# Performance work log

Measured on AMD Instinct MI355X. Metric: run time of the kernel, lower is better.

The kernel has to match this reference:

```python
import jax, jax.numpy as jnp
import numpy as np

EPS = 1e-5   # torch F.layer_norm default eps
TOP_K = 20   # int(3*D^2 / (2*hr*N^2 + 10*D)) for D=768, N=196, hr=1.0
NUM_EXPERTS = 200  # 10 * TOP_K


def setup_inputs() -> dict:
    key = jax.random.key(0)
    ks = jax.random.split(key, 6)
    B, N, D = 32, 196, 768
    E, H = NUM_EXPERTS, 196  # H = int(N * hidden_ratio)
    s = 0.02
    return {
        "x": jax.random.normal(ks[0], (B, N, D), jnp.float32),
        "Wr": jax.random.normal(ks[1], (E, D), jnp.float32) * s,   # router.weight
        "W1": jax.random.normal(ks[2], (E, H, N), jnp.float32) * s,  # fc1.weight per expert
        "b1": jnp.zeros((E, H), jnp.float32),
        "W2": jax.random.normal(ks[3], (E, N, H), jnp.float32) * s,  # fc2.weight per expert
        "b2": jnp.zeros((E, N), jnp.float32),
        "Wo": jax.random.normal(ks[4], (D, D), jnp.float32) * s,     # out_proj.weight
        "bo": jnp.zeros((D,), jnp.float32),
    }


def reference(x, Wr, W1, b1, W2, b2, Wo, bo):
    B, N, D = x.shape
    E = Wr.shape[0]
    K = TOP_K

    # Router: per-sample routing on token-mean features
    logits = x.mean(axis=1) @ Wr.T                      # (B, E)
    probs = jax.nn.softmax(logits, axis=-1)             # (B, E)
    w, idx = jax.lax.top_k(probs, K)                    # (B, K) sorted desc, as torch.topk
    w = w / w.sum(axis=-1, keepdims=True)               # renormalize top-k weights

    # TokenMixer operates in (B, D, N) space: layernorm over tokens (no affine),
    # then fc1 (N->H), gelu(tanh), fc2 (H->N).
    xt = jnp.swapaxes(x, 1, 2)                          # (B, D, N)
    mu = xt.mean(axis=-1, keepdims=True)
    var = xt.var(axis=-1, keepdims=True)                # population var (matches F.layer_norm)
    z = (xt - mu) * jax.lax.rsqrt(var + EPS)            # (B, D, N)

    # Gather each sample's K expert weight matrices and batch the MLPs.
    W1g, b1g = W1[idx], b1[idx]                         # (B,K,H,N), (B,K,H)
    W2g, b2g = W2[idx], b2[idx]                         # (B,K,N,H), (B,K,N)

    h = jnp.einsum('bdn,bkhn->bkdh', z, W1g) + b1g[:, :, None, :]
    a = jax.nn.gelu(h, approximate=True)                # tanh-approx GELU
    o = jnp.einsum('bkdh,bknh->bkdn', a, W2g) + b2g[:, :, None, :]

    # Weighted combine over the K selected experts, back to (B, N, D)
    mix = jnp.einsum('bk,bkdn->bnd', w, o)

    out = mix @ Wo.T + bo                               # out_proj

    # Load-balancing aux loss (top-1 assignment fraction vs mean router prob)
    top1 = jax.nn.one_hot(idx[:, 0], E, dtype=probs.dtype)   # (B, E)
    aux = E * jnp.sum(probs.mean(axis=0) * top1.mean(axis=0))
    return out, aux
```

## Files before the change

### kernel.cpp

```cpp
#include <hip/hip_runtime.h>
#include <math.h>

constexpr int B  = 32;
constexpr int N  = 196;
constexpr int D  = 768;
constexpr int E  = 200;
constexpr int TK = 20;

constexpr int NGRP = 4;
constexpr int PRB  = 14336;
constexpr int EXB  = 114688;
constexpr int LK   = 40;

typedef __bf16 bf16x8 __attribute__((ext_vector_type(8)));
typedef __bf16 bf16x4 __attribute__((ext_vector_type(4)));
typedef float  f32x4  __attribute__((ext_vector_type(4)));
typedef long   longx2 __attribute__((ext_vector_type(2)));
typedef unsigned char uchar;

#define GLDS16(gp, lp)                                                        \
  __builtin_amdgcn_global_load_lds(                                           \
      (const __attribute__((address_space(1))) void*)(gp),                    \
      (__attribute__((address_space(3))) void*)(lp), 16, 0, 0)

#define WAITVM8   __builtin_amdgcn_s_waitcnt(0x0F78)
#define WAITVM6   __builtin_amdgcn_s_waitcnt(0x0F76)
#define WAITVM0   __builtin_amdgcn_s_waitcnt(0x0F70)
#define WAITLGKM0 __builtin_amdgcn_s_waitcnt(0xC07F)
#define BAR       __builtin_amdgcn_s_barrier()

__device__ __forceinline__ float gelu_fast(float x) {
  float u = x * fmaf(x * x, 0.044715f, 1.0f);
  float e = exp2f(-2.3022084f * u);
  return x * __builtin_amdgcn_rcpf(1.0f + e);
}

__device__ __forceinline__ uchar f32_to_f8(float v) {
  return (uchar)(__builtin_amdgcn_cvt_pk_fp8_f32(v, v, 0, false) & 0xff);
}

__global__ __launch_bounds__(256) void k_ln(const float* __restrict__ x,
                                            uchar* __restrict__ zb,
                                            float* __restrict__ mu) {
  int b = blockIdx.x / 12, dt = blockIdx.x % 12;
  int d0 = dt * 64;
  int t = threadIdx.x;
  int q = t >> 6, d = t & 63;
  __shared__ float ps[256], pq[256];
  __shared__ float ms[64], rss[64];
  __shared__ alignas(16) uchar zt[64 * 256];

  for (int i = t; i < 1024; i += 256) ((uint4*)zt)[i] = (uint4){0, 0, 0, 0};

  const float* xp = x + ((size_t)b * N + q * 49) * D + d0 + d;
  float s = 0.f, sq = 0.f;
  #pragma unroll 7
  for (int n = 0; n < 49; ++n) {
    float v = xp[(size_t)n * D];
    s += v; sq += v * v;
  }
  ps[t] = s; pq[t] = sq;
  __syncthreads();
  if (t < 64) {
    float S = ps[t] + ps[t + 64] + ps[t + 128] + ps[t + 192];
    float Q = pq[t] + pq[t + 64] + pq[t + 128] + pq[t + 192];
    float m = S * (1.0f / N);
    float var = Q * (1.0f / N) - m * m;
    ms[t] = m; rss[t] = rsqrtf(var + 1e-5f);
    mu[(size_t)b * D + d0 + t] = m;
  }
  __syncthreads();
  float m = ms[d], r = rss[d];
  int dsw = d & 3;
  #pragma unroll 7
  for (int n = 0; n < 49; ++n) {
    float v = xp[(size_t)n * D];
    int tok = q * 49 + n;
    int qp = ((tok >> 3) & 3) ^ dsw;
    int off = d * 256 + (tok >> 6) * 64 + qp * 16 + ((tok >> 5) & 1) * 8 + (tok & 7);
    zt[off] = f32_to_f8((v - m) * r);
  }
  __syncthreads();
  #pragma unroll
  for (int pair = 0; pair < 4; ++pair) {
    uint4* dst = (uint4*)(zb + (((size_t)b * 4 + pair) * 768 + d0) * 64);
    dst[t] = ((const uint4*)zt)[(t >> 2) * 16 + pair * 4 + (t & 3)];
  }
}

__global__ __launch_bounds__(256) void k_convert(
    const float* __restrict__ W1, const float* __restrict__ W2,
    const float* __restrict__ Wo,
    uchar* __restrict__ Wf, __bf16* __restrict__ Wob) {
  int bx = blockIdx.x;
  int t = threadIdx.x;
  if (bx >= 400) {
    int i = (bx - 400) * 256 + t;
    float4 v = *(const float4*)&Wo[(size_t)i * 4];
    bf16x4 o = {(__bf16)v.x, (__bf16)v.y, (__bf16)v.z, (__bf16)v.w};
    *(bf16x4*)&Wob[(size_t)i * 4] = o;
    return;
  }
  int e = bx >> 1, mat = bx & 1;
  __shared__ alignas(16) uchar ls[224 * 256];
  for (int i = t; i < 3584; i += 256) ((uint4*)ls)[i] = (uint4){0, 0, 0, 0};
  __syncthreads();
  const float* src = (mat ? W2 : W1) + (size_t)e * 196 * 196;
  for (int i = t; i < 196 * 49; i += 256) {
    int r = i / 49, c4 = (i - r * 49) * 4;
    float4 v = *(const float4*)&src[(size_t)r * 196 + c4];
    int lo = __builtin_amdgcn_cvt_pk_fp8_f32(v.x, v.y, 0, false);
    unsigned int pk = (unsigned int)__builtin_amdgcn_cvt_pk_fp8_f32(v.z, v.w, lo, true);
    *(unsigned int*)&ls[r * 256 + c4] = pk;
  }
  __syncthreads();
  uchar* dst = Wf + (size_t)e * EXB + mat * 4 * PRB;
  for (int s = t; s < 3584; s += 256) {
    int p = s / 896, rem = s - p * 896;
    int col = rem >> 2, qp = rem & 3;
    int ql = qp ^ (col & 3);
    unsigned long lo = *(const unsigned long*)&ls[col * 256 + p * 64 + ql * 8];
    unsigned long hi = *(const unsigned long*)&ls[col * 256 + p * 64 + 32 + ql * 8];
    longx2 o; o[0] = (long)lo; o[1] = (long)hi;
    *(longx2*)&dst[(size_t)s * 16] = o;
  }
}

__global__ void k_router(const float* __restrict__ mu, const float* __restrict__ Wr,
                         float* __restrict__ probs, int* __restrict__ idxg,
                         float* __restrict__ wg) {
  int b = blockIdx.x;
  int t = threadIdx.x;
  __shared__ float smu[768];
  __shared__ float sp[E];
  __shared__ float smax, ssum;
  __shared__ float svals[TK];
  __shared__ int   sidx[TK];

  for (int i = t; i < 768; i += 256) smu[i] = mu[(size_t)b * D + i];
  __syncthreads();

  float logit = 0.f;
  if (t < E) {
    const float4* wr4 = (const float4*)(Wr + (size_t)t * D);
    const float4* m4  = (const float4*)smu;
    float acc = 0.f;
    #pragma unroll 4
    for (int i = 0; i < 192; ++i) {
      float4 w = wr4[i], m = m4[i];
      acc = fmaf(w.x, m.x, acc); acc = fmaf(w.y, m.y, acc);
      acc = fmaf(w.z, m.z, acc); acc = fmaf(w.w, m.w, acc);
    }
    logit = acc;
    sp[t] = acc;
  }
  __syncthreads();
  if (t == 0) {
    float mx = sp[0];
    for (int e = 1; e < E; ++e) mx = fmaxf(mx, sp[e]);
    smax = mx;
  }
  __syncthreads();
  if (t < E) sp[t] = expf(logit - smax);
  __syncthreads();
  if (t == 0) {
    float s = 0.f;
    for (int e = 0; e < E; ++e) s += sp[e];
    ssum = s;
  }
  __syncthreads();
  if (t < E) {
    sp[t] = sp[t] / ssum;
    probs[(size_t)b * E + t] = sp[t];
  }
  __syncthreads();

  for (int k = 0; k < TK; ++k) {
    if (t < 64) {
      float bv = -1e30f; int bi = 0;
      for (int e = t; e < E; e += 64) {
        float v = sp[e];
        if (v > bv) { bv = v; bi = e; }
      }
      #pragma unroll
      for (int off = 32; off > 0; off >>= 1) {
        float ov = __shfl_down(bv, off);
        int   oi = __shfl_down(bi, off);
        if (ov > bv || (ov == bv && oi < bi)) { bv = ov; bi = oi; }
      }
      if (t == 0) {
        svals[k] = bv; sidx[k] = bi;
        sp[bi] = -2e30f;
      }
    }
    __syncthreads();
  }
  if (t == 0) {
    float s = 0.f;
    for (int k = 0; k < TK; ++k) s += svals[k];
    float inv = 1.0f / s;
    for (int k = 0; k < TK; ++k) {
      wg[b * TK + k]   = svals[k] * inv;
      idxg[b * TK + k] = sidx[k];
    }
  }
}

__global__ __launch_bounds__(512, 1) void k_expert(
    const uchar* __restrict__ zb, const uchar* __restrict__ Wf,
    const float* __restrict__ b1, const float* __restrict__ b2,
    const int* __restrict__ idxg, const float* __restrict__ wg,
    __bf16* __restrict__ mixg) {
  __shared__ alignas(16) uchar pool[122880];
  __shared__ alignas(16) __bf16 b1s[5 * 196];
  __shared__ alignas(16) __bf16 b2s[5 * 196];
  __shared__ int   eidx_s[5];
  __shared__ float w_s[5];
  uchar* zs  = pool;
  uchar* at  = pool + 32768;
  uchar* wsb = pool + 65536;
  __bf16* tb = (__bf16*)(pool + 32768);

  int xw = blockIdx.x & 7, rr_ = blockIdx.x >> 3;
  int j = rr_ / 6, dt = rr_ - j * 6;
  int gid = j * 8 + xw;
  int g = gid & 3, b = gid >> 2;
  int d0 = dt * 128;

  int t = threadIdx.x;
  int lane = t & 63, wave = t >> 6;
  int quad = lane >> 4, l16 = lane & 15;
  int wrow = (wave & 3) * 32;
  int wcol = (wave >> 2) * 112;
  int qp = quad ^ (l16 & 3);

  if (t < 5) {
    eidx_s[t] = idxg[b * TK + g * 5 + t];
    w_s[t]    = wg[b * TK + g * 5 + t];
  }
  for (int i = t; i < 980; i += 512) {
    int kk = i / 196, col = i - kk * 196;
    int ee = idxg[b * TK + g * 5 + kk];
    b1s[i] = (__bf16)b1[ee * 196 + col];
    b2s[i] = (__bf16)b2[ee * 196 + col];
  }
  *(unsigned long*)&at[3 * 8192 + (t >> 2) * 64 + (t & 3) * 16 + 8] = 0ul;
  __syncthreads();

  {
    const uchar* zbase = zb + ((size_t)b * 4 * 768 + d0) * 64;
    #pragma unroll
    for (int p = 0; p < 4; ++p)
      GLDS16(zbase + (size_t)p * (768 * 64) + t * 16, zs + p * 8192 + t * 16);
  }

  int soff0 = t * 16;
  int soff1 = (t < 384) ? (512 + t) * 16 : (t - 384) * 16;

  auto issue = [&](int qn) {
    int qq = qn > 39 ? 39 : qn;
    int kk2 = qq >> 3, rem = qq & 7;
    const uchar* src = Wf + (size_t)eidx_s[kk2] * EXB + rem * PRB;
    uchar* lb = wsb + (qn & 3) * PRB;
    GLDS16(src + soff0, lb + soff0);
    GLDS16(src + soff1, lb + soff1);
  };
  issue(0); issue(1); issue(2); issue(3);

  WAITVM8;
  BAR;
  longx2 zf[4][2];
  #pragma unroll
  for (int p = 0; p < 4; ++p) {
    zf[p][0] = *(const longx2*)&zs[p * 8192 + (wrow + l16) * 64 + qp * 16];
    zf[p][1] = *(const longx2*)&zs[p * 8192 + (wrow + 16 + l16) * 64 + qp * 16];
  }

  f32x4 macc[14];
  #pragma unroll
  for (int i = 0; i < 14; ++i) macc[i] = (f32x4){0.f, 0.f, 0.f, 0.f};

  #pragma unroll 1
  for (int kk = 0; kk < 5; ++kk) {
    float wkv = w_s[kk];
    f32x4 hacc[14];
    #pragma unroll
    for (int i = 0; i < 14; ++i) hacc[i] = (f32x4){0.f, 0.f, 0.f, 0.f};

    #pragma unroll 1
    for (int p = 0; p < 4; ++p) {
      int q = kk * 8 + p;
      WAITVM6;
      BAR;
      const uchar* buf = wsb + (q & 3) * PRB;
      #pragma unroll
      for (int ct = 0; ct < 7; ++ct) {
        longx2 bf = *(const longx2*)&buf[(wcol + ct * 16 + l16) * 64 + qp * 16];
        hacc[ct]     = __builtin_amdgcn_mfma_f32_16x16x32_fp8_fp8(bf[0], zf[p][0][0], hacc[ct], 0, 0, 0);
        hacc[ct]     = __builtin_amdgcn_mfma_f32_16x16x32_fp8_fp8(bf[1], zf[p][0][1], hacc[ct], 0, 0, 0);
        hacc[7 + ct] = __builtin_amdgcn_mfma_f32_16x16x32_fp8_fp8(bf[0], zf[p][1][0], hacc[7 + ct], 0, 0, 0);
        hacc[7 + ct] = __builtin_amdgcn_mfma_f32_16x16x32_fp8_fp8(bf[1], zf[p][1][1], hacc[7 + ct], 0, 0, 0);
      }
      BAR;
      issue(q + 4);
    }

    #pragma unroll
    for (int ct = 0; ct < 7; ++ct) {
      int hb = wcol + ct * 16 + quad * 4;
      bool valid = hb < 196;
      unsigned pk0 = 0u, pk1 = 0u;
      if (valid) {
        bf16x4 b4 = *(const bf16x4*)&b1s[kk * 196 + hb];
        float bv0 = (float)b4[0], bv1 = (float)b4[1];
        float bv2 = (float)b4[2], bv3 = (float)b4[3];
        f32x4 h0 = hacc[ct], h1 = hacc[7 + ct];
        pk0 = (unsigned)__builtin_amdgcn_cvt_pk_fp8_f32(
                  gelu_fast(h0[0] + bv0) * wkv, gelu_fast(h0[1] + bv1) * wkv, 0, false);
        pk0 = (unsigned)__builtin_amdgcn_cvt_pk_fp8_f32(
                  gelu_fast(h0[2] + bv2) * wkv, gelu_fast(h0[3] + bv3) * wkv, (int)pk0, true);
        pk1 = (unsigned)__builtin_amdgcn_cvt_pk_fp8_f32(
                  gelu_fast(h1[0] + bv0) * wkv, gelu_fast(h1[1] + bv1) * wkv, 0, false);
        pk1 = (unsigned)__builtin_amdgcn_cvt_pk_fp8_f32(
                  gelu_fast(h1[2] + bv2) * wkv, gelu_fast(h1[3] + bv3) * wkv, (int)pk1, true);
      }
      int d0r = wrow + l16;
      int addr0 = (hb >> 6) * 8192 + d0r * 64 + ((((hb >> 3) & 3) ^ (d0r & 3)) << 4)
                + ((hb >> 5) & 1) * 8 + (quad & 1) * 4;
      *(unsigned*)&at[addr0]        = pk0;
      *(unsigned*)&at[addr0 + 1024] = pk1;
    }
    WAITLGKM0;

    #pragma unroll 1
    for (int p = 0; p < 4; ++p) {
      int q = kk * 8 + 4 + p;
      WAITVM6;
      BAR;
      const uchar* buf = wsb + (q & 3) * PRB;
      longx2 a0 = *(const longx2*)&at[p * 8192 + (wrow + l16) * 64 + qp * 16];
      longx2 a1 = *(const longx2*)&at[p * 8192 + (wrow + 16 + l16) * 64 + qp * 16];
      #pragma unroll
      for (int ct = 0; ct < 7; ++ct) {
        longx2 bf = *(const longx2*)&buf[(wcol + ct * 16 + l16) * 64 + qp * 16];
        macc[ct]     = __builtin_amdgcn_mfma_f32_16x16x32_fp8_fp8(a0[0], bf[0], macc[ct], 0, 0, 0);
        macc[ct]     = __builtin_amdgcn_mfma_f32_16x16x32_fp8_fp8(a0[1], bf[1], macc[ct], 0, 0, 0);
        macc[7 + ct] = __builtin_amdgcn_mfma_f32_16x16x32_fp8_fp8(a1[0], bf[0], macc[7 + ct], 0, 0, 0);
        macc[7 + ct] = __builtin_amdgcn_mfma_f32_16x16x32_fp8_fp8(a1[1], bf[1], macc[7 + ct], 0, 0, 0);
      }
      BAR;
      issue(q + 4);
    }
  }

  WAITVM0;
  BAR;
  #pragma unroll
  for (int ct = 0; ct < 7; ++ct) {
    int ncol = wcol + ct * 16 + l16;
    float bsum = 0.f;
    if (ncol < 196) {
      #pragma unroll
      for (int k5 = 0; k5 < 5; ++k5)
        bsum += w_s[k5] * (float)b2s[k5 * 196 + ncol];
    }
    #pragma unroll
    for (int rt = 0; rt < 2; ++rt) {
      f32x4 v = macc[rt * 7 + ct];
      bf16x4 o = {(__bf16)(v[0] + bsum), (__bf16)(v[1] + bsum),
                  (__bf16)(v[2] + bsum), (__bf16)(v[3] + bsum)};
      *(bf16x4*)&tb[ncol * 132 + wrow + rt * 16 + quad * 4] = o;
    }
  }
  __syncthreads();
  __bf16* mp = mixg + ((size_t)(g * B + b) * N) * D + d0;
  #pragma unroll
  for (int i = 0; i < 7; ++i) {
    int s = i * 512 + t;
    if (s < 3136) {
      int n = s >> 4, c = s & 15;
      const uint2* pa = (const uint2*)&tb[n * 132 + c * 8];
      uint2 v0 = pa[0], v1 = pa[1];
      uint4 v = {v0.x, v0.y, v1.x, v1.y};
      *(uint4*)&mp[(size_t)n * D + c * 8] = v;
    }
  }
}

__global__ __launch_bounds__(256, 2) void k_outproj(
    const __bf16* __restrict__ mixg, const __bf16* __restrict__ Wob,
    const float* __restrict__ bo, const float* __restrict__ probs,
    const int* __restrict__ idxg, float* __restrict__ out,
    float* __restrict__ out_aux) {
  __shared__ alignas(16) __bf16 As[64 * LK];
  __shared__ alignas(16) __bf16 Bs[256 * LK];
  const size_t GS = (size_t)B * N * D;

  int t = threadIdx.x;
  if (blockIdx.x == 0 && t < 32) {
    int top1 = idxg[t * TK];
    float s = 0.f;
    for (int bb = 0; bb < B; ++bb) s += probs[(size_t)bb * E + top1];
    #pragma unroll
    for (int off = 16; off > 0; off >>= 1) s += __shfl_down(s, off);
    if (t == 0) out_aux[0] = s * ((float)E / ((float)B * (float)B));
  }

  int m0 = (blockIdx.x % 98) * 64;
  int e0 = (blockIdx.x / 98) * 256;
  int lane = t & 63, wave = t >> 6;
  int quad = lane >> 4, l16 = lane & 15;
  int wrow = (wave & 1) * 32;
  int wcol = (wave >> 1) * 128;
  int arow = t >> 2, ach = t & 3;
  const __bf16* ap0 = mixg + (size_t)(m0 + arow) * D + ach * 8;

  f32x4 acc[16];
  #pragma unroll
  for (int i = 0; i < 16; ++i) acc[i] = (f32x4){0.f, 0.f, 0.f, 0.f};

  const uint4* wsrc = (const uint4*)Wob;
  #pragma unroll 1
  for (int c = 0; c < 24; ++c) {
    int k0 = c * 32;
    __syncthreads();
    {
      const __bf16* ap = ap0 + k0;
      bf16x8 g0 = *(const bf16x8*)(ap);
      bf16x8 g1 = *(const bf16x8*)(ap + GS);
      bf16x8 g2 = *(const bf16x8*)(ap + 2 * GS);
      bf16x8 g3 = *(const bf16x8*)(ap + 3 * GS);
      bf16x8 r;
      #pragma unroll
      for (int jj = 0; jj < 8; ++jj)
        r[jj] = (__bf16)((float)g0[jj] + (float)g1[jj] + (float)g2[jj] + (float)g3[jj]);
      *(bf16x8*)&As[arow * LK + ach * 8] = r;
    }
    for (int p = t; p < 1024; p += 256) {
      int rr = p >> 2, sub = p & 3;
      uint4 v = wsrc[(((size_t)(e0 + rr)) * D + k0) / 8 + sub];
      *(uint4*)&Bs[rr * LK + sub * 8] = v;
    }
    __syncthreads();
    bf16x8 a0 = *(const bf16x8*)&As[(wrow + l16) * LK + quad * 8];
    bf16x8 a1 = *(const bf16x8*)&As[(wrow + 16 + l16) * LK + quad * 8];
    #pragma unroll
    for (int ct = 0; ct < 8; ++ct) {
      bf16x8 bfr = *(const bf16x8*)&Bs[(wcol + ct * 16 + l16) * LK + quad * 8];
      acc[ct]     = __builtin_amdgcn_mfma_f32_16x16x32_bf16(a0, bfr, acc[ct], 0, 0, 0);
      acc[8 + ct] = __builtin_amdgcn_mfma_f32_16x16x32_bf16(a1, bfr, acc[8 + ct], 0, 0, 0);
    }
  }

  #pragma unroll
  for (int ct = 0; ct < 8; ++ct) {
    int e = e0 + wcol + ct * 16 + l16;
    float bov = bo[e];
    #pragma unroll
    for (int rt = 0; rt < 2; ++rt) {
      #pragma unroll
      for (int rx = 0; rx < 4; ++rx) {
        int m = m0 + wrow + rt * 16 + quad * 4 + rx;
        out[(size_t)m * D + e] = acc[rt * 8 + ct][rx] + bov;
      }
    }
  }
}

extern "C" void kernel_launch(void* const* d_in, const int* in_sizes, int n_in,
                              void* d_out, int out_size, void* d_ws, size_t ws_size,
                              hipStream_t stream) {
  const float* x  = (const float*)d_in[0];
  const float* Wr = (const float*)d_in[1];
  const float* W1 = (const float*)d_in[2];
  const float* b1 = (const float*)d_in[3];
  const float* W2 = (const float*)d_in[4];
  const float* b2 = (const float*)d_in[5];
  const float* Wo = (const float*)d_in[6];
  const float* bo = (const float*)d_in[7];
  float* out = (float*)d_out;

  char* p = (char*)d_ws;
  auto alloc = [&](size_t bytes) {
    char* r = p;
    p += (bytes + 255) & ~(size_t)255;
    return r;
  };
  uchar*  zb   = (uchar*)alloc((size_t)B * 4 * 768 * 64);
  float*  mu   = (float*)alloc((size_t)B * D * 4);
  uchar*  Wf   = (uchar*)alloc((size_t)E * EXB);
  __bf16* Wob  = (__bf16*)alloc((size_t)D * D * 2);
  __bf16* mixg = (__bf16*)alloc((size_t)NGRP * B * N * D * 2);
  float*  probs= (float*)alloc((size_t)B * E * 4);
  int*    idxg = (int*)alloc((size_t)B * TK * 4);
  float*  wg   = (float*)alloc((size_t)B * TK * 4);

  k_ln<<<dim3(B * 12), dim3(256), 0, stream>>>(x, zb, mu);
  k_convert<<<dim3(976), dim3(256), 0, stream>>>(W1, W2, Wo, Wf, Wob);
  k_router<<<dim3(B), dim3(256), 0, stream>>>(mu, Wr, probs, idxg, wg);
  k_expert<<<dim3(768), dim3(512), 0, stream>>>(zb, Wf, b1, b2, idxg, wg, mixg);
  k_outproj<<<dim3(294), dim3(256), 0, stream>>>(mixg, Wob, bo, probs, idxg,
                                                 out, out + (size_t)B * N * D);
}
```

Baseline: 412.7 us.

## Halve expert d-tile, triple-buffer weight stages, run two blocks per CU

The expert kernel moves from 512-thread blocks covering 128 d-rows with a 4-deep weight ring to 256-thread blocks covering 64 d-rows with a 3-deep ring. The grid doubles to 1536 blocks and launch bounds allow two blocks per CU. LDS per block shrinks so two blocks can be resident, with the aim of better latency hiding and load balance. The LDS swizzle changes from (row&3) to ((row>>1)&3), and the LN and convert kernels are updated to match. The trade-off is that each expert weight tile is now fetched twice as often, because each block covers half as many d-rows.

```diff
diff --git a/kernel.cpp b/kernel.cpp
--- a/kernel.cpp
+++ b/kernel.cpp
@@ -23,8 +23,8 @@
       (const __attribute__((address_space(1))) void*)(gp),                    \
       (__attribute__((address_space(3))) void*)(lp), 16, 0, 0)
 
+#define WAITVM12  __builtin_amdgcn_s_waitcnt(0x0F7C)
 #define WAITVM8   __builtin_amdgcn_s_waitcnt(0x0F78)
-#define WAITVM6   __builtin_amdgcn_s_waitcnt(0x0F76)
 #define WAITVM0   __builtin_amdgcn_s_waitcnt(0x0F70)
 #define WAITLGKM0 __builtin_amdgcn_s_waitcnt(0xC07F)
 #define BAR       __builtin_amdgcn_s_barrier()
@@ -71,7 +71,7 @@
   }
   __syncthreads();
   float m = ms[d], r = rss[d];
-  int dsw = d & 3;
+  int dsw = (d >> 1) & 3;
   #pragma unroll 7
   for (int n = 0; n < 49; ++n) {
     float v = xp[(size_t)n * D];
@@ -118,7 +118,7 @@
   for (int s = t; s < 3584; s += 256) {
     int p = s / 896, rem = s - p * 896;
     int col = rem >> 2, qp = rem & 3;
-    int ql = qp ^ (col & 3);
+    int ql = qp ^ ((col >> 1) & 3);
     unsigned long lo = *(const unsigned long*)&ls[col * 256 + p * 64 + ql * 8];
     unsigned long hi = *(const unsigned long*)&ls[col * 256 + p * 64 + 32 + ql * 8];
     longx2 o; o[0] = (long)lo; o[1] = (long)hi;
@@ -206,74 +206,76 @@
   }
 }
 
-__global__ __launch_bounds__(512, 1) void k_expert(
+__global__ __launch_bounds__(256, 2) void k_expert(
     const uchar* __restrict__ zb, const uchar* __restrict__ Wf,
     const float* __restrict__ b1, const float* __restrict__ b2,
     const int* __restrict__ idxg, const float* __restrict__ wg,
     __bf16* __restrict__ mixg) {
-  __shared__ alignas(16) uchar pool[122880];
+  __shared__ alignas(16) uchar pool[75776];
   __shared__ alignas(16) __bf16 b1s[5 * 196];
   __shared__ alignas(16) __bf16 b2s[5 * 196];
   __shared__ int   eidx_s[5];
   __shared__ float w_s[5];
   uchar* zs  = pool;
-  uchar* at  = pool + 32768;
-  uchar* wsb = pool + 65536;
-  __bf16* tb = (__bf16*)(pool + 32768);
+  uchar* at  = pool + 16384;
+  uchar* wsb = pool + 32768;
+  __bf16* tb = (__bf16*)pool;
 
   int xw = blockIdx.x & 7, rr_ = blockIdx.x >> 3;
-  int j = rr_ / 6, dt = rr_ - j * 6;
+  int j = rr_ / 12, dt = rr_ - j * 12;
   int gid = j * 8 + xw;
   int g = gid & 3, b = gid >> 2;
-  int d0 = dt * 128;
+  int d0 = dt * 64;
 
   int t = threadIdx.x;
   int lane = t & 63, wave = t >> 6;
   int quad = lane >> 4, l16 = lane & 15;
-  int wrow = (wave & 3) * 32;
-  int wcol = (wave >> 2) * 112;
-  int qp = quad ^ (l16 & 3);
+  int wrow = (wave & 1) * 32;
+  int wcol = (wave >> 1) * 112;
+  int qp = quad ^ ((l16 >> 1) & 3);
 
   if (t < 5) {
     eidx_s[t] = idxg[b * TK + g * 5 + t];
     w_s[t]    = wg[b * TK + g * 5 + t];
   }
-  for (int i = t; i < 980; i += 512) {
+  for (int i = t; i < 980; i += 256) {
     int kk = i / 196, col = i - kk * 196;
     int ee = idxg[b * TK + g * 5 + kk];
     b1s[i] = (__bf16)b1[ee * 196 + col];
     b2s[i] = (__bf16)b2[ee * 196 + col];
   }
-  *(unsigned long*)&at[3 * 8192 + (t >> 2) * 64 + (t & 3) * 16 + 8] = 0ul;
+  *(unsigned long*)&at[3 * 4096 + (t >> 2) * 64 + (t & 3) * 16 + 8] = 0ul;
   __syncthreads();
 
   {
     const uchar* zbase = zb + ((size_t)b * 4 * 768 + d0) * 64;
     #pragma unroll
     for (int p = 0; p < 4; ++p)
-      GLDS16(zbase + (size_t)p * (768 * 64) + t * 16, zs + p * 8192 + t * 16);
-  }
-
-  int soff0 = t * 16;
-  int soff1 = (t < 384) ? (512 + t) * 16 : (t - 384) * 16;
+      GLDS16(zbase + (size_t)p * (768 * 64) + t * 16, zs + p * 4096 + t * 16);
+  }
+
+  int s0 = t * 16, s1 = (t + 256) * 16, s2 = (t + 512) * 16;
+  int s3 = ((t & 127) + 768) * 16;
 
   auto issue = [&](int qn) {
     int qq = qn > 39 ? 39 : qn;
     int kk2 = qq >> 3, rem = qq & 7;
     const uchar* src = Wf + (size_t)eidx_s[kk2] * EXB + rem * PRB;
-    uchar* lb = wsb + (qn & 3) * PRB;
-    GLDS16(src + soff0, lb + soff0);
-    GLDS16(src + soff1, lb + soff1);
+    uchar* lb = wsb + (qn % 3) * PRB;
+    GLDS16(src + s0, lb + s0);
+    GLDS16(src + s1, lb + s1);
+    GLDS16(src + s2, lb + s2);
+    GLDS16(src + s3, lb + s3);
   };
-  issue(0); issue(1); issue(2); issue(3);
-
-  WAITVM8;
+  issue(0); issue(1); issue(2);
+
+  WAITVM12;
   BAR;
   longx2 zf[4][2];
   #pragma unroll
   for (int p = 0; p < 4; ++p) {
-    zf[p][0] = *(const longx2*)&zs[p * 8192 + (wrow + l16) * 64 + qp * 16];
-    zf[p][1] = *(const longx2*)&zs[p * 8192 + (wrow + 16 + l16) * 64 + qp * 16];
+    zf[p][0] = *(const longx2*)&zs[p * 4096 + (wrow + l16) * 64 + qp * 16];
+    zf[p][1] = *(const longx2*)&zs[p * 4096 + (wrow + 16 + l16) * 64 + qp * 16];
   }
 
   f32x4 macc[14];
@@ -290,9 +292,9 @@
     #pragma unroll 1
     for (int p = 0; p < 4; ++p) {
       int q = kk * 8 + p;
-      WAITVM6;
+      WAITVM8;
       BAR;
-      const uchar* buf = wsb + (q & 3) * PRB;
+      const uchar* buf = wsb + (q % 3) * PRB;
       #pragma unroll
       for (int ct = 0; ct < 7; ++ct) {
         longx2 bf = *(const longx2*)&buf[(wcol + ct * 16 + l16) * 64 + qp * 16];
@@ -302,7 +304,7 @@
         hacc[7 + ct] = __builtin_amdgcn_mfma_f32_16x16x32_fp8_fp8(bf[1], zf[p][1][1], hacc[7 + ct], 0, 0, 0);
       }
       BAR;
-      issue(q + 4);
+      issue(q + 3);
     }
 
     #pragma unroll
@@ -325,7 +327,7 @@
                   gelu_fast(h1[2] + bv2) * wkv, gelu_fast(h1[3] + bv3) * wkv, (int)pk1, true);
       }
       int d0r = wrow + l16;
-      int addr0 = (hb >> 6) * 8192 + d0r * 64 + ((((hb >> 3) & 3) ^ (d0r & 3)) << 4)
+      int addr0 = (hb >> 6) * 4096 + d0r * 64 + ((((hb >> 3) & 3) ^ ((d0r >> 1) & 3)) << 4)
                 + ((hb >> 5) & 1) * 8 + (quad & 1) * 4;
       *(unsigned*)&at[addr0]        = pk0;
       *(unsigned*)&at[addr0 + 1024] = pk1;
@@ -335,11 +337,11 @@
     #pragma unroll 1
     for (int p = 0; p < 4; ++p) {
       int q = kk * 8 + 4 + p;
-      WAITVM6;
+      WAITVM8;
       BAR;
-      const uchar* buf = wsb + (q & 3) * PRB;
-      longx2 a0 = *(const longx2*)&at[p * 8192 + (wrow + l16) * 64 + qp * 16];
-      longx2 a1 = *(const longx2*)&at[p * 8192 + (wrow + 16 + l16) * 64 + qp * 16];
+      const uchar* buf = wsb + (q % 3) * PRB;
+      longx2 a0 = *(const longx2*)&at[p * 4096 + (wrow + l16) * 64 + qp * 16];
+      longx2 a1 = *(const longx2*)&at[p * 4096 + (wrow + 16 + l16) * 64 + qp * 16];
       #pragma unroll
       for (int ct = 0; ct < 7; ++ct) {
         longx2 bf = *(const longx2*)&buf[(wcol + ct * 16 + l16) * 64 + qp * 16];
@@ -349,7 +351,7 @@
         macc[7 + ct] = __builtin_amdgcn_mfma_f32_16x16x32_fp8_fp8(a1[1], bf[1], macc[7 + ct], 0, 0, 0);
       }
       BAR;
-      issue(q + 4);
+      issue(q + 3);
     }
   }
 
@@ -369,17 +371,17 @@
       f32x4 v = macc[rt * 7 + ct];
       bf16x4 o = {(__bf16)(v[0] + bsum), (__bf16)(v[1] + bsum),
                   (__bf16)(v[2] + bsum), (__bf16)(v[3] + bsum)};
-      *(bf16x4*)&tb[ncol * 132 + wrow + rt * 16 + quad * 4] = o;
+      *(bf16x4*)&tb[ncol * 68 + wrow + rt * 16 + quad * 4] = o;
     }
   }
   __syncthreads();
   __bf16* mp = mixg + ((size_t)(g * B + b) * N) * D + d0;
   #pragma unroll
   for (int i = 0; i < 7; ++i) {
-    int s = i * 512 + t;
-    if (s < 3136) {
-      int n = s >> 4, c = s & 15;
-      const uint2* pa = (const uint2*)&tb[n * 132 + c * 8];
+    int s = i * 256 + t;
+    if (s < 1568) {
+      int n = s >> 3, c = s & 7;
+      const uint2* pa = (const uint2*)&tb[n * 68 + c * 8];
       uint2 v0 = pa[0], v1 = pa[1];
       uint4 v = {v0.x, v0.y, v1.x, v1.y};
       *(uint4*)&mp[(size_t)n * D + c * 8] = v;
@@ -498,7 +500,7 @@
   k_ln<<<dim3(B * 12), dim3(256), 0, stream>>>(x, zb, mu);
   k_convert<<<dim3(976), dim3(256), 0, stream>>>(W1, W2, Wo, Wf, Wob);
   k_router<<<dim3(B), dim3(256), 0, stream>>>(mu, Wr, probs, idxg, wg);
-  k_expert<<<dim3(768), dim3(512), 0, stream>>>(zb, Wf, b1, b2, idxg, wg, mixg);
+  k_expert<<<dim3(1536), dim3(256), 0, stream>>>(zb, Wf, b1, b2, idxg, wg, mixg);
   k_outproj<<<dim3(294), dim3(256), 0, stream>>>(mixg, Wob, bo, probs, idxg,
                                                  out, out + (size_t)B * N * D);
 }
```

Result: faster. 394.9 us (-4.3%).
